# Kernel tuning notes

Hardware: AMD Instinct MI355X
Metric: run time of the kernel (lower is better)

The kernel has to match this reference:

```python
import jax, jax.numpy as jnp
import numpy as np

BLOCK_SIZE = 128  # config.block_size; first query block skips intra-block causal mask (faithful to source)
NEG = -1e9       # the module uses -1e9, not -inf, for masking and m_i init


def setup_inputs() -> dict:
    key = jax.random.key(0)
    kq, kk, kv, km = jax.random.split(key, 4)
    B, S, H, D = 2, 2048, 16, 64
    q = jax.random.normal(kq, (B, S, H, D), dtype=jnp.float32)
    k = jax.random.normal(kk, (B, S, H, D), dtype=jnp.float32)
    v = jax.random.normal(kv, (B, S, H, D), dtype=jnp.float32)
    mask = jax.random.randint(km, (B, S), 0, 2).astype(bool)
    mask = mask.at[:, 0].set(True)  # keep first key attendable
    return {"q": q, "k": k, "v": v, "mask": mask}


def reference(q, k, v, mask):
    # q,k,v: [B,S,H,D]; mask: [B,S] bool (True = attend)
    B, S, H, D = q.shape
    scale = 1.0 / np.sqrt(D)
    # config.normalize_query=True -> F.normalize(q, dim=-1) (eps=1e-12)
    qn = q / jnp.maximum(jnp.linalg.norm(q, axis=-1, keepdims=True), 1e-12)
    # scores: [B,S(query),H,S(key)]
    scores = jnp.einsum('bshd,bkhd->bshk', qn, k) * scale
    qi = jnp.arange(S)[:, None]
    ki = jnp.arange(S)[None, :]
    # Faithful causal structure of the blocked PyTorch fallback:
    #  - keys limited to k <= q (triu(diagonal=block_start+1) masking)
    #  - EXCEPT the first query block (block_start==0), where the intra-block
    #    causal mask is skipped (keys still limited to the first block).
    allowed = (ki <= qi) | ((qi < BLOCK_SIZE) & (ki < BLOCK_SIZE))  # [S,S]
    scores = jnp.where(allowed[None, :, None, :], scores, NEG)
    scores = jnp.where(mask[:, None, None, :], scores, NEG)
    p = jax.nn.softmax(scores, axis=-1)
    out = jnp.einsum('bshk,bkhd->bshd', p, v)
    return out
```

## Files before the change

### kernel.cpp

```cpp
#include <hip/hip_runtime.h>
#include <stdint.h>

typedef __attribute__((ext_vector_type(8))) short short8;
typedef __attribute__((ext_vector_type(4))) float floatx4;
typedef __attribute__((ext_vector_type(4))) unsigned int uintx4;
typedef __attribute__((ext_vector_type(2))) unsigned int uintx2;

#define S_LEN 2048
#define NHEAD 16
#define DHEAD 64
#define KB    64
#define NTILE 32
#define PL_BYTES (S_LEN * DHEAD * 2)
#define VOFF  (2 * NHEAD * PL_BYTES)
#define MOFF  (2 * VOFF)
#define WS_NEEDED ((size_t)MOFF + 2 * 4096)
#define NEGINF (-__builtin_inff())
#define LOG2E 1.4426950408889634f

#define GLOAD_LDS16(gp, lp) \
    __builtin_amdgcn_global_load_lds((const __attribute__((address_space(1))) unsigned int*)(gp), \
                                     (__attribute__((address_space(3))) unsigned int*)(lp), 16, 0, 0)

static __device__ __forceinline__ unsigned f2bf(float f) {
    union { float f; unsigned u; } w; w.f = f;
    return (w.u + 0x7FFFu + ((w.u >> 16) & 1u)) >> 16;
}

static __device__ __forceinline__ unsigned cvtpk(float lo, float hi) {
    unsigned r;
    asm("v_cvt_pk_bf16_f32 %0, %1, %2" : "=v"(r) : "v"(lo), "v"(hi));
    return r;
}

static __device__ __forceinline__ floatx4 mfma16(short8 a, short8 b, floatx4 c) {
    return __builtin_amdgcn_mfma_f32_16x16x32_bf16(a, b, c, 0, 0, 0);
}

__global__ __launch_bounds__(256) void prep_kernel(
    const float* __restrict__ kg, const float* __restrict__ vg,
    const int* __restrict__ mg, char* __restrict__ ws)
{
    __shared__ unsigned short Tl[64 * 72];
    const int bid = blockIdx.x;
    const int t   = bid & 31;
    const int bh  = bid >> 5;
    const int b   = bh >> 4, h = bh & 15;
    const int tid = threadIdx.x;
    char* kpre = ws + (size_t)bh * PL_BYTES;
    char* vpre = ws + VOFF + (size_t)bh * PL_BYTES;

    {
        const int r  = tid >> 2;
        const int c0 = (tid & 3) * 32;
        const int X  = (r & 7) << 4;
        const size_t grow = (((size_t)b * S_LEN + t * 64 + r) * NHEAD + h) * DHEAD;
        #pragma unroll
        for (int cc = 0; cc < 2; ++cc) {
            const int c  = c0 + 16 * cc;
            const int d0 = (c ^ X) >> 1;
            floatx4 f0 = *(const floatx4*)(kg + grow + d0);
            floatx4 f1 = *(const floatx4*)(kg + grow + d0 + 4);
            uintx4 pk = (uintx4){ f2bf(f0[0]) | (f2bf(f0[1]) << 16),
                                  f2bf(f0[2]) | (f2bf(f0[3]) << 16),
                                  f2bf(f1[0]) | (f2bf(f1[1]) << 16),
                                  f2bf(f1[2]) | (f2bf(f1[3]) << 16) };
            *(uintx4*)(kpre + t * 8192 + r * 128 + c) = pk;
        }
    }
    {
        const int key = tid >> 2;
        const int d0  = (tid & 3) * 16;
        const float vz = mg[(size_t)b * S_LEN + t * 64 + key] ? 1.f : 0.f;
        const size_t grow = (((size_t)b * S_LEN + t * 64 + key) * NHEAD + h) * DHEAD;
        #pragma unroll
        for (int q = 0; q < 4; ++q) {
            floatx4 f = *(const floatx4*)(vg + grow + d0 + 4 * q);
            #pragma unroll
            for (int ii = 0; ii < 4; ++ii)
                Tl[(d0 + 4 * q + ii) * 72 + key] = (unsigned short)f2bf(f[ii] * vz);
        }
    }
    __syncthreads();
    {
        const int d  = tid >> 2;
        const int c0 = (tid & 3) * 32;
        const int Xv = (d & 7) << 4;
        #pragma unroll
        for (int cc = 0; cc < 2; ++cc) {
            const int c   = c0 + 16 * cc;
            const int pp0 = (c ^ Xv) >> 1;
            const int blk = pp0 >> 5;
            const int a   = (pp0 & 31) >> 3;
            unsigned short vals[8];
            #pragma unroll
            for (int i = 0; i < 8; ++i) {
                const int key = 32 * blk + ((i < 4) ? (4 * a + i) : (16 + 4 * a + i - 4));
                vals[i] = Tl[d * 72 + key];
            }
            *(uintx4*)(vpre + t * 8192 + d * 128 + c) = *(const uintx4*)vals;
        }
    }
    if (h == 0 && tid < 64) {
        const int key = tid;
        const int gg = (key >> 2) & 3, lo = key & 3;
        const int ks = key >> 5,      hi = (key >> 4) & 1;
        const unsigned short mv = mg[(size_t)b * S_LEN + t * 64 + key] ? 0x3F80 : 0;
        *(unsigned short*)(ws + MOFF + (size_t)b * 4096 + t * 128
                           + gg * 32 + ks * 16 + (4 * hi + lo) * 2) = mv;
    }
}

__global__ __launch_bounds__(512, 4) void fa3_main(
    const float* __restrict__ qg, const char* __restrict__ ws,
    float* __restrict__ og)
{
    __shared__ char smem[65536];
    unsigned short* Qs = (unsigned short*)smem;
    char* KsB = smem + 16384;
    char* VsB = smem + 40960;

    const int tid  = threadIdx.x;
    const int bid  = blockIdx.x;
    const int b    = bid >> 8;
    const int bh   = (b << 4) | (bid & 15);
    const int rpair= (bid >> 4) & 15;
    const int qb   = b ? rpair : 15 - rpair;
    const int h    = bh & 15;
    const int w    = tid >> 6;
    const int lane = tid & 63;
    const int g    = lane >> 4;
    const int lm   = lane & 15;
    const int kh   = w >> 2;
    const int wq   = w & 3;
    const char* kpre = ws + (size_t)bh * PL_BYTES;
    const char* vpre = ws + VOFF + (size_t)bh * PL_BYTES;
    const char* mgf  = ws + MOFF + (size_t)b * 4096;
    const int nkt = (qb == 0) ? 2 : (2 * qb + 2);

    GLOAD_LDS16(kpre + tid * 16, KsB + tid * 16);
    GLOAD_LDS16(vpre + tid * 16, VsB + tid * 16);

    {
        const int r  = tid >> 2;
        const int q0 = tid & 3;
        const float* src = qg + (((size_t)b * S_LEN + (size_t)qb * 128 + r) * NHEAD + h) * DHEAD + q0 * 16;
        floatx4 f0 = *(const floatx4*)(src + 0);
        floatx4 f1 = *(const floatx4*)(src + 4);
        floatx4 f2 = *(const floatx4*)(src + 8);
        floatx4 f3 = *(const floatx4*)(src + 12);
        float ssq = 0.f;
        #pragma unroll
        for (int i = 0; i < 4; ++i)
            ssq += f0[i]*f0[i] + f1[i]*f1[i] + f2[i]*f2[i] + f3[i]*f3[i];
        ssq += __shfl_xor(ssq, 1);
        ssq += __shfl_xor(ssq, 2);
        const float sc = (0.125f * LOG2E) / fmaxf(sqrtf(ssq), 1e-12f);
        float fv[16];
        #pragma unroll
        for (int i = 0; i < 4; ++i) { fv[i]=f0[i]; fv[4+i]=f1[i]; fv[8+i]=f2[i]; fv[12+i]=f3[i]; }
        unsigned pk[8];
        #pragma unroll
        for (int i = 0; i < 8; ++i)
            pk[i] = cvtpk(fv[2*i]*sc, fv[2*i+1]*sc);
        const int X = (r & 7) << 4;
        char* qp = (char*)Qs + r * 128;
        *(uintx4*)(qp + ((32*q0)      ^ X)) = (uintx4){pk[0],pk[1],pk[2],pk[3]};
        *(uintx4*)(qp + ((32*q0 + 16) ^ X)) = (uintx4){pk[4],pk[5],pk[6],pk[7]};
    }
    __syncthreads();

    const int Xl = (lm & 7) << 4;
    short8 qf[2][2];
    #pragma unroll
    for (int grp = 0; grp < 2; ++grp) {
        const int row = wq * 32 + grp * 16 + lm;
        const char* base = (const char*)Qs + row * 128;
        #pragma unroll
        for (int ksd = 0; ksd < 2; ++ksd)
            qf[grp][ksd] = *(const short8*)(base + ((64*ksd + 16*g) ^ Xl));
    }

    short8 mfn = *(const short8*)(mgf + 0 * 128 + g * 32 + kh * 16);
    if (nkt > 1) {
        GLOAD_LDS16(kpre + 8192 + tid * 16, KsB + 8192 + tid * 16);
        GLOAD_LDS16(vpre + 8192 + tid * 16, VsB + 8192 + tid * 16);
    }

    floatx4 oacc[2][4];
    floatx4 dacc[2];
    #pragma unroll
    for (int grp = 0; grp < 2; ++grp) {
        dacc[grp] = (floatx4){0.f,0.f,0.f,0.f};
        #pragma unroll
        for (int nt = 0; nt < 4; ++nt) oacc[grp][nt] = (floatx4){0.f,0.f,0.f,0.f};
    }
    floatx4 NEG8 = (floatx4){-8.f,-8.f,-8.f,-8.f};
    asm volatile("" : "+v"(NEG8));
    const int qgl0 = qb * 128 + wq * 32 + lm;

    int cur = 0;
    for (int kt = 0; kt < nkt; ++kt) {
        if (kt + 1 < nkt) { asm volatile("s_waitcnt vmcnt(2)" ::: "memory"); }
        else              { asm volatile("s_waitcnt vmcnt(0)" ::: "memory"); }
        __builtin_amdgcn_s_barrier();
        __builtin_amdgcn_sched_barrier(0);

        const short8 mf = mfn;
        if (kt + 1 < nkt)
            mfn = *(const short8*)(mgf + (kt + 1) * 128 + g * 32 + kh * 16);
        if (kt + 2 < nkt) {
            int nb = cur + 2; if (nb >= 3) nb -= 3;
            const size_t tb = (size_t)(kt + 2) * 8192;
            GLOAD_LDS16(kpre + tb + tid * 16, KsB + nb * 8192 + tid * 16);
            GLOAD_LDS16(vpre + tb + tid * 16, VsB + nb * 8192 + tid * 16);
        }

        floatx4 st[2][2];
        const char* kbase = KsB + cur * 8192 + kh * 4096 + lm * 128;
        __builtin_amdgcn_s_setprio(1);
        #pragma unroll
        for (int mt = 0; mt < 2; ++mt) {
            short8 kf = *(const short8*)(kbase + mt * 2048 + ((16*g) ^ Xl));
            st[0][mt] = mfma16(kf, qf[0][0], NEG8);
            st[1][mt] = mfma16(kf, qf[1][0], NEG8);
        }
        #pragma unroll
        for (int mt = 0; mt < 2; ++mt) {
            short8 kf = *(const short8*)(kbase + mt * 2048 + ((64 + 16*g) ^ Xl));
            st[0][mt] = mfma16(kf, qf[0][1], st[0][mt]);
            st[1][mt] = mfma16(kf, qf[1][1], st[1][mt]);
        }
        __builtin_amdgcn_s_setprio(0);

        if ((qb >= 1) && (kt >= 2 * qb)) {
            #pragma unroll
            for (int mt = 0; mt < 2; ++mt)
                #pragma unroll
                for (int j = 0; j < 4; ++j) {
                    const int kgl = kt * KB + kh * 32 + mt * 16 + 4 * g + j;
                    if (kgl > qgl0)      st[0][mt][j] = -10000.f;
                    if (kgl > qgl0 + 16) st[1][mt][j] = -10000.f;
                }
        }

        short8 pa[2];
        #pragma unroll
        for (int grp = 0; grp < 2; ++grp) {
            float p[8];
            #pragma unroll
            for (int mt = 0; mt < 2; ++mt)
                #pragma unroll
                for (int j = 0; j < 4; ++j)
                    p[mt * 4 + j] = exp2f(st[grp][mt][j]);
            union { short8 s; uintx4 u; } pu;
            pu.u = (uintx4){ cvtpk(p[0], p[1]), cvtpk(p[2], p[3]),
                             cvtpk(p[4], p[5]), cvtpk(p[6], p[7]) };
            pa[grp] = pu.s;
        }
        __builtin_amdgcn_s_setprio(1);
        dacc[0] = mfma16(pa[0], mf, dacc[0]);
        dacc[1] = mfma16(pa[1], mf, dacc[1]);
        {
            const char* vbase = VsB + cur * 8192 + lm * 128;
            #pragma unroll
            for (int nt = 0; nt < 4; ++nt) {
                short8 vf = *(const short8*)(vbase + nt * 2048 + ((64*kh + 16*g) ^ Xl));
                oacc[0][nt] = mfma16(pa[0], vf, oacc[0][nt]);
                oacc[1][nt] = mfma16(pa[1], vf, oacc[1][nt]);
            }
        }
        __builtin_amdgcn_s_setprio(0);

        cur += 1; if (cur >= 3) cur -= 3;
    }
    __syncthreads();

    floatx4* rbuf = (floatx4*)(smem + 16384);
    float*   dbuf = (float*)smem;
    if (kh == 1) {
        #pragma unroll
        for (int grp = 0; grp < 2; ++grp)
            #pragma unroll
            for (int nt = 0; nt < 4; ++nt)
                rbuf[((grp * 4 + nt) * 4 + wq) * 64 + lane] = oacc[grp][nt];
    }
    __syncthreads();
    if (kh == 0) {
        #pragma unroll
        for (int grp = 0; grp < 2; ++grp)
            #pragma unroll
            for (int nt = 0; nt < 4; ++nt)
                oacc[grp][nt] += rbuf[((grp * 4 + nt) * 4 + wq) * 64 + lane];
    }
    __syncthreads();
    if (kh == 1 && lm == 0) {
        #pragma unroll
        for (int grp = 0; grp < 2; ++grp)
            #pragma unroll
            for (int j = 0; j < 4; ++j)
                dbuf[wq * 32 + grp * 16 + 4 * g + j] = dacc[grp][j];
    }
    __syncthreads();
    if (kh == 0) {
        #pragma unroll
        for (int grp = 0; grp < 2; ++grp)
            #pragma unroll
            for (int j = 0; j < 4; ++j) {
                const float den = dacc[grp][j] + dbuf[wq * 32 + grp * 16 + 4 * g + j];
                const float invj = 1.0f / den;
                const int row = qb * 128 + wq * 32 + grp * 16 + 4 * g + j;
                float* dst = og + (((size_t)b * S_LEN + row) * NHEAD + h) * DHEAD + lm;
                #pragma unroll
                for (int nt = 0; nt < 4; ++nt) dst[nt * 16] = oacc[grp][nt][j] * invj;
            }
    }
}

__global__ __launch_bounds__(512) void fa3_fallback(
    const float* __restrict__ qg, const float* __restrict__ kg,
    const float* __restrict__ vg, const int* __restrict__ mg,
    float* __restrict__ og)
{
    __shared__ unsigned short Qs[128 * DHEAD];
    __shared__ unsigned short Ks2[KB * DHEAD];
    __shared__ unsigned short Vt[DHEAD * KB];
    __shared__ float Ms[KB];

    const int tid  = threadIdx.x;
    const int bid  = blockIdx.x;
    const int qb   = 15 - (bid >> 5);
    const int bh   = bid & 31;
    const int b    = bh >> 4;
    const int h    = bh & 15;
    const int w    = tid >> 6;
    const int lane = tid & 63;
    const int g    = lane >> 4;
    const int lm   = lane & 15;

    {
        const int r  = tid >> 2;
        const int q0 = tid & 3;
        const float* src = qg + (((size_t)b * S_LEN + (size_t)qb * 128 + r) * NHEAD + h) * DHEAD + q0 * 16;
        floatx4 f0 = *(const floatx4*)(src + 0);
        floatx4 f1 = *(const floatx4*)(src + 4);
        floatx4 f2 = *(const floatx4*)(src + 8);
        floatx4 f3 = *(const floatx4*)(src + 12);
        float ssq = 0.f;
        #pragma unroll
        for (int i = 0; i < 4; ++i)
            ssq += f0[i]*f0[i] + f1[i]*f1[i] + f2[i]*f2[i] + f3[i]*f3[i];
        ssq += __shfl_xor(ssq, 1);
        ssq += __shfl_xor(ssq, 2);
        const float sc = 0.125f / fmaxf(sqrtf(ssq), 1e-12f);
        float fv[16];
        #pragma unroll
        for (int i = 0; i < 4; ++i) { fv[i]=f0[i]; fv[4+i]=f1[i]; fv[8+i]=f2[i]; fv[12+i]=f3[i]; }
        unsigned pk[8];
        #pragma unroll
        for (int i = 0; i < 8; ++i)
            pk[i] = f2bf(fv[2*i]*sc) | (f2bf(fv[2*i+1]*sc) << 16);
        const int X = (r & 7) << 4;
        char* qp = (char*)Qs + r * 128;
        *(uintx4*)(qp + ((32*q0)      ^ X)) = (uintx4){pk[0],pk[1],pk[2],pk[3]};
        *(uintx4*)(qp + ((32*q0 + 16) ^ X)) = (uintx4){pk[4],pk[5],pk[6],pk[7]};
    }
    __syncthreads();

    short8 qf[2];
    {
        const int row = w * 16 + lm;
        const int X = (row & 7) << 4;
        const char* base = (const char*)Qs + row * 128;
        #pragma unroll
        for (int ks = 0; ks < 2; ++ks) {
            union { short8 s; uintx2 u[2]; } u;
            u.u[0] = *(const uintx2*)(base + ((64*ks + 8*g)      ^ X));
            u.u[1] = *(const uintx2*)(base + ((64*ks + 8*g + 32) ^ X));
            qf[ks] = u.s;
        }
    }

    floatx4 oacc[4];
    #pragma unroll
    for (int nt = 0; nt < 4; ++nt) oacc[nt] = (floatx4){0.f,0.f,0.f,0.f};
    float mrun = NEGINF, lrun = 0.f;
    const int q_glob = qb * 128 + w * 16 + lm;
    const int nkt = (qb == 0) ? 2 : (2 * qb + 2);

    for (int kt = 0; kt < nkt; ++kt) {
        const int kb0 = kt * KB;
        {
            const int r = tid >> 3;
            const int o = tid & 7;
            const size_t goff = (((size_t)b * S_LEN + kb0 + r) * NHEAD + h) * DHEAD + o * 8;
            floatx4 a0 = *(const floatx4*)(kg + goff);
            floatx4 a1 = *(const floatx4*)(kg + goff + 4);
            floatx4 c0 = *(const floatx4*)(vg + goff);
            floatx4 c1 = *(const floatx4*)(vg + goff + 4);
            uintx4 kw = (uintx4){ f2bf(a0[0]) | (f2bf(a0[1])<<16),
                                  f2bf(a0[2]) | (f2bf(a0[3])<<16),
                                  f2bf(a1[0]) | (f2bf(a1[1])<<16),
                                  f2bf(a1[2]) | (f2bf(a1[3])<<16) };
            *(uintx4*)((char*)Ks2 + r*128 + ((16*o) ^ ((r & 7) << 4))) = kw;
            float cv[8];
            #pragma unroll
            for (int i = 0; i < 4; ++i) { cv[i] = c0[i]; cv[4+i] = c1[i]; }
            #pragma unroll
            for (int i = 0; i < 8; ++i) {
                const int d = 8*o + i;
                Vt[d*64 + (r ^ (((i ^ o) & 7) << 3))] = (unsigned short)f2bf(cv[i]);
            }
            if (tid < KB) Ms[tid] = mg[(size_t)b * S_LEN + kb0 + tid] ? 0.f : NEGINF;
        }
        __syncthreads();

        floatx4 st[4];
        #pragma unroll
        for (int mt = 0; mt < 4; ++mt) st[mt] = (floatx4){0.f,0.f,0.f,0.f};
        #pragma unroll
        for (int ks = 0; ks < 2; ++ks) {
            #pragma unroll
            for (int mt = 0; mt < 4; ++mt) {
                const int row = mt * 16 + lm;
                const int X = (row & 7) << 4;
                const char* base = (const char*)Ks2 + row * 128;
                union { short8 s; uintx2 u[2]; } u;
                u.u[0] = *(const uintx2*)(base + ((64*ks + 8*g)      ^ X));
                u.u[1] = *(const uintx2*)(base + ((64*ks + 8*g + 32) ^ X));
                st[mt] = mfma16(u.s, qf[ks], st[mt]);
            }
        }

        const bool diag = (qb > 0) && (kt >= 2 * qb);
        float sv[16];
        #pragma unroll
        for (int mt = 0; mt < 4; ++mt) {
            #pragma unroll
            for (int j = 0; j < 4; ++j) {
                const int kl = mt * 16 + 4 * g + j;
                float s = st[mt][j] + Ms[kl];
                if (diag && (kb0 + kl > q_glob)) s = NEGINF;
                sv[mt * 4 + j] = s;
            }
        }

        float rmax = sv[0];
        #pragma unroll
        for (int i = 1; i < 16; ++i) rmax = fmaxf(rmax, sv[i]);
        rmax = fmaxf(rmax, __shfl_xor(rmax, 16));
        rmax = fmaxf(rmax, __shfl_xor(rmax, 32));
        const float mnew = fmaxf(mrun, rmax);
        const float cf = __expf(mrun - mnew);
        float p[16], psum = 0.f;
        #pragma unroll
        for (int i = 0; i < 16; ++i) { p[i] = __expf(sv[i] - mnew); psum += p[i]; }
        psum += __shfl_xor(psum, 16);
        psum += __shfl_xor(psum, 32);
        lrun = lrun * cf + psum;
        mrun = mnew;

        float cj[4];
        #pragma unroll
        for (int j = 0; j < 4; ++j) cj[j] = __shfl(cf, 20 * g + j);
        #pragma unroll
        for (int nt = 0; nt < 4; ++nt)
            #pragma unroll
            for (int j = 0; j < 4; ++j) oacc[nt][j] *= cj[j];

        short8 pa[2];
        #pragma unroll
        for (int ks = 0; ks < 2; ++ks)
            #pragma unroll
            for (int i = 0; i < 8; ++i)
                pa[ks][i] = (short)f2bf(p[(2*ks + (i>>2))*4 + (i&3)]);

        #pragma unroll
        for (int nt = 0; nt < 4; ++nt) {
            const int d = 16 * nt + lm;
            const int xz = (((d & 7) ^ ((d >> 3) & 7)) & 7) << 4;
            const char* vb = (const char*)Vt + d * 128;
            #pragma unroll
            for (int ks = 0; ks < 2; ++ks) {
                union { short8 s; uintx2 u[2]; } vu;
                vu.u[0] = *(const uintx2*)(vb + ((64*ks + 8*g)      ^ xz));
                vu.u[1] = *(const uintx2*)(vb + ((64*ks + 8*g + 32) ^ xz));
                oacc[nt] = mfma16(pa[ks], vu.s, oacc[nt]);
            }
        }
        __syncthreads();
    }

    const float inv = 1.0f / lrun;
    #pragma unroll
    for (int j = 0; j < 4; ++j) {
        const float invj = __shfl(inv, 20 * g + j);
        const int row = qb * 128 + w * 16 + 4 * g + j;
        float* dst = og + (((size_t)b * S_LEN + row) * NHEAD + h) * DHEAD + lm;
        #pragma unroll
        for (int nt = 0; nt < 4; ++nt) dst[nt * 16] = oacc[nt][j] * invj;
    }
}

extern "C" void kernel_launch(void* const* d_in, const int* in_sizes, int n_in,
                              void* d_out, int out_size, void* d_ws, size_t ws_size,
                              hipStream_t stream)
{
    const float* q = (const float*)d_in[0];
    const float* k = (const float*)d_in[1];
    const float* v = (const float*)d_in[2];
    const int*   m = (const int*)d_in[3];
    float* out = (float*)d_out;
    (void)in_sizes; (void)n_in; (void)out_size;
    if (ws_size >= WS_NEEDED) {
        prep_kernel<<<dim3(1024), dim3(256), 0, stream>>>(k, v, m, (char*)d_ws);
        fa3_main<<<dim3(512), dim3(512), 0, stream>>>(q, (const char*)d_ws, out);
    } else {
        fa3_fallback<<<dim3(512), dim3(512), 0, stream>>>(q, k, v, m, out);
    }
}
```

Baseline: 51.28 us.

## Split long causal query blocks across key chunks with separate combine pass

Query blocks shrink from 128 to 64 rows with 256-thread workgroups. The longest half of the query blocks have their key range split into two chunks processed by separate workgroups, which write partial numerators and denominators to workspace; a new combine kernel sums and normalizes them. The K/V pipeline changes from triple buffering with one barrier per tile to double buffering with a full vmcnt(0) wait and syncthreads per tile. The aim is to balance the triangular causal workload across more workgroups and reduce tail imbalance, at the cost of an extra kernel launch, workspace traffic and a less overlapped load pipeline.

```diff
diff --git a/kernel.cpp b/kernel.cpp
--- a/kernel.cpp
+++ b/kernel.cpp
@@ -14,7 +14,9 @@
 #define PL_BYTES (S_LEN * DHEAD * 2)
 #define VOFF  (2 * NHEAD * PL_BYTES)
 #define MOFF  (2 * VOFF)
-#define WS_NEEDED ((size_t)MOFF + 2 * 4096)
+#define POFF  (MOFF + 8192)
+#define DOFF  (POFF + 1024 * 16384)
+#define WS_NEEDED ((size_t)DOFF + 1024 * 256)
 #define NEGINF (-__builtin_inff())
 #define LOG2E 1.4426950408889634f
 
@@ -111,40 +113,52 @@
     }
 }
 
-__global__ __launch_bounds__(512, 4) void fa3_main(
-    const float* __restrict__ qg, const char* __restrict__ ws,
+__global__ __launch_bounds__(256, 4) void fa3_main(
+    const float* __restrict__ qg, char* __restrict__ ws,
     float* __restrict__ og)
 {
-    __shared__ char smem[65536];
+    __shared__ char smem[40960];
     unsigned short* Qs = (unsigned short*)smem;
-    char* KsB = smem + 16384;
-    char* VsB = smem + 40960;
+    char* KsB = smem + 8192;
+    char* VsB = smem + 24576;
 
     const int tid  = threadIdx.x;
     const int bid  = blockIdx.x;
-    const int b    = bid >> 8;
-    const int bh   = (b << 4) | (bid & 15);
-    const int rpair= (bid >> 4) & 15;
-    const int qb   = b ? rpair : 15 - rpair;
+    int a, bh, chunk;
+    if (bid < 1024) { a = 31 - (bid >> 6); chunk = (bid >> 5) & 1; bh = bid & 31; }
+    else            { int r = bid - 1024; a = 15 - (r >> 5); chunk = 0; bh = r & 31; }
+    const int b    = bh >> 4;
     const int h    = bh & 15;
     const int w    = tid >> 6;
     const int lane = tid & 63;
     const int g    = lane >> 4;
     const int lm   = lane & 15;
-    const int kh   = w >> 2;
-    const int wq   = w & 3;
+    const int kh   = w >> 1;
+    const int wq   = w & 1;
     const char* kpre = ws + (size_t)bh * PL_BYTES;
     const char* vpre = ws + VOFF + (size_t)bh * PL_BYTES;
     const char* mgf  = ws + MOFF + (size_t)b * 4096;
-    const int nkt = (qb == 0) ? 2 : (2 * qb + 2);
-
-    GLOAD_LDS16(kpre + tid * 16, KsB + tid * 16);
-    GLOAD_LDS16(vpre + tid * 16, VsB + tid * 16);
+
+    const int nktTot = (a < 2) ? 2 : (a + 1);
+    const bool split = (a >= 16);
+    int kt0, kt1;
+    if (split) {
+        const int h1 = nktTot >> 1, h0 = nktTot - h1;
+        kt0 = chunk ? h0 : 0;  kt1 = chunk ? nktTot : h0;
+    } else { kt0 = 0; kt1 = nktTot; }
+
+    {
+        const size_t tb = (size_t)kt0 * 8192;
+        GLOAD_LDS16(kpre + tb + tid * 16,        KsB + tid * 16);
+        GLOAD_LDS16(kpre + tb + 4096 + tid * 16, KsB + 4096 + tid * 16);
+        GLOAD_LDS16(vpre + tb + tid * 16,        VsB + tid * 16);
+        GLOAD_LDS16(vpre + tb + 4096 + tid * 16, VsB + 4096 + tid * 16);
+    }
 
     {
         const int r  = tid >> 2;
         const int q0 = tid & 3;
-        const float* src = qg + (((size_t)b * S_LEN + (size_t)qb * 128 + r) * NHEAD + h) * DHEAD + q0 * 16;
+        const float* src = qg + (((size_t)b * S_LEN + (size_t)a * 64 + r) * NHEAD + h) * DHEAD + q0 * 16;
         floatx4 f0 = *(const floatx4*)(src + 0);
         floatx4 f1 = *(const floatx4*)(src + 4);
         floatx4 f2 = *(const floatx4*)(src + 8);
@@ -168,6 +182,7 @@
         *(uintx4*)(qp + ((32*q0)      ^ X)) = (uintx4){pk[0],pk[1],pk[2],pk[3]};
         *(uintx4*)(qp + ((32*q0 + 16) ^ X)) = (uintx4){pk[4],pk[5],pk[6],pk[7]};
     }
+    asm volatile("s_waitcnt vmcnt(0)" ::: "memory");
     __syncthreads();
 
     const int Xl = (lm & 7) << 4;
@@ -181,12 +196,6 @@
             qf[grp][ksd] = *(const short8*)(base + ((64*ksd + 16*g) ^ Xl));
     }
 
-    short8 mfn = *(const short8*)(mgf + 0 * 128 + g * 32 + kh * 16);
-    if (nkt > 1) {
-        GLOAD_LDS16(kpre + 8192 + tid * 16, KsB + 8192 + tid * 16);
-        GLOAD_LDS16(vpre + 8192 + tid * 16, VsB + 8192 + tid * 16);
-    }
-
     floatx4 oacc[2][4];
     floatx4 dacc[2];
     #pragma unroll
@@ -197,24 +206,20 @@
     }
     floatx4 NEG8 = (floatx4){-8.f,-8.f,-8.f,-8.f};
     asm volatile("" : "+v"(NEG8));
-    const int qgl0 = qb * 128 + wq * 32 + lm;
+    const int qgl0 = a * 64 + wq * 32 + lm;
 
     int cur = 0;
-    for (int kt = 0; kt < nkt; ++kt) {
-        if (kt + 1 < nkt) { asm volatile("s_waitcnt vmcnt(2)" ::: "memory"); }
-        else              { asm volatile("s_waitcnt vmcnt(0)" ::: "memory"); }
-        __builtin_amdgcn_s_barrier();
-        __builtin_amdgcn_sched_barrier(0);
-
-        const short8 mf = mfn;
-        if (kt + 1 < nkt)
-            mfn = *(const short8*)(mgf + (kt + 1) * 128 + g * 32 + kh * 16);
-        if (kt + 2 < nkt) {
-            int nb = cur + 2; if (nb >= 3) nb -= 3;
-            const size_t tb = (size_t)(kt + 2) * 8192;
-            GLOAD_LDS16(kpre + tb + tid * 16, KsB + nb * 8192 + tid * 16);
-            GLOAD_LDS16(vpre + tb + tid * 16, VsB + nb * 8192 + tid * 16);
-        }
+    for (int kt = kt0; kt < kt1; ++kt) {
+        if (kt + 1 < kt1) {
+            const size_t tb = (size_t)(kt + 1) * 8192;
+            char* kb = KsB + (cur ^ 1) * 8192;
+            char* vb = VsB + (cur ^ 1) * 8192;
+            GLOAD_LDS16(kpre + tb + tid * 16,        kb + tid * 16);
+            GLOAD_LDS16(kpre + tb + 4096 + tid * 16, kb + 4096 + tid * 16);
+            GLOAD_LDS16(vpre + tb + tid * 16,        vb + tid * 16);
+            GLOAD_LDS16(vpre + tb + 4096 + tid * 16, vb + 4096 + tid * 16);
+        }
+        const short8 mf = *(const short8*)(mgf + kt * 128 + g * 32 + kh * 16);
 
         floatx4 st[2][2];
         const char* kbase = KsB + cur * 8192 + kh * 4096 + lm * 128;
@@ -233,7 +238,7 @@
         }
         __builtin_amdgcn_s_setprio(0);
 
-        if ((qb >= 1) && (kt >= 2 * qb)) {
+        if ((a >= 2) && (kt == a)) {
             #pragma unroll
             for (int mt = 0; mt < 2; ++mt)
                 #pragma unroll
@@ -272,18 +277,19 @@
         }
         __builtin_amdgcn_s_setprio(0);
 
-        cur += 1; if (cur >= 3) cur -= 3;
-    }
-    __syncthreads();
-
-    floatx4* rbuf = (floatx4*)(smem + 16384);
+        asm volatile("s_waitcnt vmcnt(0)" ::: "memory");
+        __syncthreads();
+        cur ^= 1;
+    }
+
+    floatx4* rbuf = (floatx4*)(smem + 8192);
     float*   dbuf = (float*)smem;
     if (kh == 1) {
         #pragma unroll
         for (int grp = 0; grp < 2; ++grp)
             #pragma unroll
             for (int nt = 0; nt < 4; ++nt)
-                rbuf[((grp * 4 + nt) * 4 + wq) * 64 + lane] = oacc[grp][nt];
+                rbuf[((grp * 4 + nt) * 2 + wq) * 64 + lane] = oacc[grp][nt];
     }
     __syncthreads();
     if (kh == 0) {
@@ -291,7 +297,7 @@
         for (int grp = 0; grp < 2; ++grp)
             #pragma unroll
             for (int nt = 0; nt < 4; ++nt)
-                oacc[grp][nt] += rbuf[((grp * 4 + nt) * 4 + wq) * 64 + lane];
+                oacc[grp][nt] += rbuf[((grp * 4 + nt) * 2 + wq) * 64 + lane];
     }
     __syncthreads();
     if (kh == 1 && lm == 0) {
@@ -303,18 +309,58 @@
     }
     __syncthreads();
     if (kh == 0) {
-        #pragma unroll
-        for (int grp = 0; grp < 2; ++grp)
-            #pragma unroll
-            for (int j = 0; j < 4; ++j) {
-                const float den = dacc[grp][j] + dbuf[wq * 32 + grp * 16 + 4 * g + j];
-                const float invj = 1.0f / den;
-                const int row = qb * 128 + wq * 32 + grp * 16 + 4 * g + j;
-                float* dst = og + (((size_t)b * S_LEN + row) * NHEAD + h) * DHEAD + lm;
+        if (!split) {
+            #pragma unroll
+            for (int grp = 0; grp < 2; ++grp)
                 #pragma unroll
-                for (int nt = 0; nt < 4; ++nt) dst[nt * 16] = oacc[grp][nt][j] * invj;
-            }
-    }
+                for (int j = 0; j < 4; ++j) {
+                    const int rl = wq * 32 + grp * 16 + 4 * g + j;
+                    const float invj = 1.0f / (dacc[grp][j] + dbuf[rl]);
+                    float* dst = og + (((size_t)b * S_LEN + a * 64 + rl) * NHEAD + h) * DHEAD + lm;
+                    #pragma unroll
+                    for (int nt = 0; nt < 4; ++nt) dst[nt * 16] = oacc[grp][nt][j] * invj;
+                }
+        } else {
+            const int s = (((a & 15) * 32 + bh) << 1) | chunk;
+            float* po = (float*)(ws + POFF + (size_t)s * 16384);
+            float* pd = (float*)(ws + DOFF + (size_t)s * 256);
+            #pragma unroll
+            for (int grp = 0; grp < 2; ++grp)
+                #pragma unroll
+                for (int j = 0; j < 4; ++j) {
+                    const int rl = wq * 32 + grp * 16 + 4 * g + j;
+                    #pragma unroll
+                    for (int nt = 0; nt < 4; ++nt)
+                        po[rl * 64 + nt * 16 + lm] = oacc[grp][nt][j];
+                    if (lm == 0) pd[rl] = dacc[grp][j] + dbuf[rl];
+                }
+        }
+    }
+}
+
+__global__ __launch_bounds__(256) void fa3_combine(
+    const char* __restrict__ ws, float* __restrict__ og)
+{
+    const int i0  = (blockIdx.x * 256 + threadIdx.x) * 8;
+    const int d   = i0 & 63;
+    const int row = (i0 >> 6) & 63;
+    const int bh  = (i0 >> 12) & 31;
+    const int ai  = i0 >> 17;
+    const int b   = bh >> 4, h = bh & 15;
+    const int s0  = ((ai * 32 + bh) << 1);
+    const float* p0 = (const float*)(ws + POFF + (size_t)s0 * 16384) + row * 64 + d;
+    const float* p1 = (const float*)(ws + POFF + (size_t)(s0 + 1) * 16384) + row * 64 + d;
+    const float den = ((const float*)(ws + DOFF + (size_t)s0 * 256))[row]
+                    + ((const float*)(ws + DOFF + (size_t)(s0 + 1) * 256))[row];
+    const float inv = 1.0f / den;
+    floatx4 a0 = *(const floatx4*)p0, a1 = *(const floatx4*)(p0 + 4);
+    floatx4 b0 = *(const floatx4*)p1, b1 = *(const floatx4*)(p1 + 4);
+    floatx4 o0, o1;
+    #pragma unroll
+    for (int i = 0; i < 4; ++i) { o0[i] = (a0[i] + b0[i]) * inv; o1[i] = (a1[i] + b1[i]) * inv; }
+    float* dst = og + (((size_t)b * S_LEN + (16 + ai) * 64 + row) * NHEAD + h) * DHEAD + d;
+    *(floatx4*)dst       = o0;
+    *(floatx4*)(dst + 4) = o1;
 }
 
 __global__ __launch_bounds__(512) void fa3_fallback(
@@ -514,7 +560,8 @@
     (void)in_sizes; (void)n_in; (void)out_size;
     if (ws_size >= WS_NEEDED) {
         prep_kernel<<<dim3(1024), dim3(256), 0, stream>>>(k, v, m, (char*)d_ws);
-        fa3_main<<<dim3(512), dim3(512), 0, stream>>>(q, (const char*)d_ws, out);
+        fa3_main<<<dim3(1536), dim3(256), 0, stream>>>(q, (char*)d_ws, out);
+        fa3_combine<<<dim3(1024), dim3(256), 0, stream>>>((const char*)d_ws, out);
     } else {
         fa3_fallback<<<dim3(512), dim3(512), 0, stream>>>(q, k, v, m, out);
     }
```

New measurement: 52.66 us. 2.7% more time.
